# Performance work log

Hardware: AMD Instinct MI355X
Metric: run time of the kernel (lower is better)

The kernel has to match this reference:

```python
import jax, jax.numpy as jnp
import numpy as np

B, P, H, W = 64, 50000, 512, 512


def setup_inputs() -> dict:
    key = jax.random.key(0)
    ks = jax.random.split(key, 6)
    x = jax.random.normal(ks[0], (B, 1, H, W), dtype=jnp.float32)
    x_A = jax.random.randint(ks[1], (B, P), 0, W, dtype=jnp.int32)
    y_A = jax.random.randint(ks[2], (B, P), 0, H, dtype=jnp.int32)
    x_B = jax.random.randint(ks[3], (B, P), 0, W, dtype=jnp.int32)
    y_B = jax.random.randint(ks[4], (B, P), 0, H, dtype=jnp.int32)
    # ordinal relation in {-1, 0, 1}: -1/+1 = ordered pair, 0 = equal depth
    gt = jax.random.randint(ks[5], (B, P), -1, 2).astype(jnp.float32)
    return {"x": x, "x_A": x_A, "y_A": y_A, "x_B": x_B, "y_B": y_B, "gt": gt}


def reference(x, x_A, y_A, x_B, y_B, gt):
    # x: [B,1,H,W] predicted depth; gather z values at sparse point pairs.
    img = x[:, 0]                              # [B,H,W]
    b = jnp.arange(B)[:, None]                 # [B,1] batch index for gather
    z_A = img[b, y_A, x_A]                     # [B,P]
    z_B = img[b, y_B, x_B]                     # [B,P]
    d = z_A - z_B
    mask = jnp.abs(gt)                         # 1 for ordered pairs, 0 for equal
    # ranking loss log(1+exp(-gt*d)) for ordered pairs, (d)^2 for equal pairs
    loss = mask * jnp.log1p(jnp.exp(-gt * d)) + (1.0 - mask) * d * d
    n_point_total = B * P
    return jnp.sum(loss) / n_point_total
```

## Files before the change

### kernel.cpp

```cpp
#include <hip/hip_runtime.h>

#define THREADS 256
#define BLOCKS_PER_XCD 391
#define NXCD 8
#define NBLOCKS (BLOCKS_PER_XCD * NXCD)

typedef int   intx4   __attribute__((ext_vector_type(4)));
typedef float floatx4 __attribute__((ext_vector_type(4)));

__global__ __launch_bounds__(THREADS) void rdc_kernel(
    const float* __restrict__ x,
    const int*   __restrict__ xA,
    const int*   __restrict__ yA,
    const int*   __restrict__ xB,
    const int*   __restrict__ yB,
    const float* __restrict__ gt,
    float* __restrict__ out,
    float inv_n)
{
    const int UPB = 12500;
    const int HW  = 512 * 512;

    const int xcd = blockIdx.x & 7;
    const int lb  = blockIdx.x >> 3;
    const int tlocal = lb * THREADS + threadIdx.x;

    float acc = 0.0f;
    if (tlocal < 8 * UPB) {
        const int bl = tlocal / UPB;
        const int i  = tlocal - bl * UPB;
        const int b  = xcd * 8 + bl;
        const int v  = b * UPB + i;

        const intx4  xa = __builtin_nontemporal_load((const intx4*)xA + v);
        const intx4  ya = __builtin_nontemporal_load((const intx4*)yA + v);
        const intx4  xb = __builtin_nontemporal_load((const intx4*)xB + v);
        const intx4  yb = __builtin_nontemporal_load((const intx4*)yB + v);
        const floatx4 g = __builtin_nontemporal_load((const floatx4*)gt + v);

        const float* __restrict__ img = x + (size_t)b * HW;

        float zA[4], zB[4];
        #pragma unroll
        for (int k = 0; k < 4; ++k) {
            zA[k] = img[(ya[k] << 9) + xa[k]];
            zB[k] = img[(yb[k] << 9) + xb[k]];
        }

        #pragma unroll
        for (int k = 0; k < 4; ++k) {
            float gi = g[k];
            float d  = zA[k] - zB[k];
            float t  = -gi * d;
            float sp = fmaxf(t, 0.0f) + log1pf(__expf(-fabsf(t)));
            float m  = fabsf(gi);
            acc += m * sp + (1.0f - m) * d * d;
        }
    }

    #pragma unroll
    for (int off = 32; off > 0; off >>= 1)
        acc += __shfl_down(acc, off, 64);

    __shared__ float wsum[THREADS / 64];
    const int lane = threadIdx.x & 63;
    const int wid  = threadIdx.x >> 6;
    if (lane == 0) wsum[wid] = acc;
    __syncthreads();
    if (threadIdx.x == 0) {
        float s = 0.0f;
        #pragma unroll
        for (int i2 = 0; i2 < THREADS / 64; ++i2) s += wsum[i2];
        atomicAdd(out, s * inv_n);
    }
}

extern "C" void kernel_launch(void* const* d_in, const int* in_sizes, int n_in,
                              void* d_out, int out_size, void* d_ws, size_t ws_size,
                              hipStream_t stream) {
    const float* x  = (const float*)d_in[0];
    const int*   xA = (const int*)d_in[1];
    const int*   yA = (const int*)d_in[2];
    const int*   xB = (const int*)d_in[3];
    const int*   yB = (const int*)d_in[4];
    const float* gt = (const float*)d_in[5];
    float* out = (float*)d_out;

    const int n = in_sizes[1];
    const float inv_n = 1.0f / (float)n;

    hipMemsetAsync(out, 0, sizeof(float), stream);
    rdc_kernel<<<NBLOCKS, THREADS, 0, stream>>>(x, xA, yA, xB, yB, gt, out, inv_n);
}
```

Before: 172.9 us.

## Stage image bands in LDS and resolve gathers from shared memory

```diff
diff --git a/kernel.cpp b/kernel.cpp
--- a/kernel.cpp
+++ b/kernel.cpp
@@ -1,14 +1,13 @@
 #include <hip/hip_runtime.h>
 
-#define THREADS 256
-#define BLOCKS_PER_XCD 391
-#define NXCD 8
-#define NBLOCKS (BLOCKS_PER_XCD * NXCD)
+#define THREADS 1024
+#define PPT 16
+#define CPB (THREADS * PPT)
+#define NCHUNK 4
+#define NBANDS 16
+#define BAND_F (32 * 512)
 
-typedef int   intx4   __attribute__((ext_vector_type(4)));
-typedef float floatx4 __attribute__((ext_vector_type(4)));
-
-__global__ __launch_bounds__(THREADS) void rdc_kernel(
+__global__ __launch_bounds__(THREADS, 4) void rdc_kernel(
     const float* __restrict__ x,
     const int*   __restrict__ xA,
     const int*   __restrict__ yA,
@@ -18,59 +17,76 @@
     float* __restrict__ out,
     float inv_n)
 {
-    const int UPB = 12500;
-    const int HW  = 512 * 512;
+    __shared__ float band[BAND_F];
+    __shared__ float wsum[THREADS / 64];
 
+    const int tid = threadIdx.x;
     const int xcd = blockIdx.x & 7;
-    const int lb  = blockIdx.x >> 3;
-    const int tlocal = lb * THREADS + threadIdx.x;
+    const int w   = blockIdx.x >> 3;
+    const int bl  = w >> 2;
+    const int ch  = w & 3;
+    const int b   = xcd * 8 + bl;
+    const int base = ch * CPB;
+    const int cnt  = min(CPB, 50000 - base);
+
+    const size_t pbase = (size_t)b * 50000 + base;
+
+    unsigned pa[PPT], pb[PPT];
+    float g[PPT], zA[PPT], zB[PPT];
+    #pragma unroll
+    for (int k = 0; k < PPT; ++k) {
+        const int s = k * THREADS + tid;
+        if (s < cnt) {
+            const size_t p = pbase + s;
+            const int xa_ = __builtin_nontemporal_load(xA + p);
+            const int ya_ = __builtin_nontemporal_load(yA + p);
+            const int xb_ = __builtin_nontemporal_load(xB + p);
+            const int yb_ = __builtin_nontemporal_load(yB + p);
+            g[k]  = __builtin_nontemporal_load(gt + p);
+            pa[k] = (unsigned)((ya_ << 9) | xa_);
+            pb[k] = (unsigned)((yb_ << 9) | xb_);
+        } else {
+            pa[k] = 0xFFFFFFFFu; pb[k] = 0xFFFFFFFFu; g[k] = 0.0f;
+        }
+        zA[k] = 0.0f; zB[k] = 0.0f;
+    }
+
+    const float4* __restrict__ img4 = (const float4*)(x + (size_t)b * (512 * 512));
+
+    for (int bi = 0; bi < NBANDS; ++bi) {
+        __syncthreads();
+        float4* dst4 = (float4*)band;
+        #pragma unroll
+        for (int j = 0; j < BAND_F / 4 / THREADS; ++j)
+            dst4[j * THREADS + tid] = img4[bi * (BAND_F / 4) + j * THREADS + tid];
+        __syncthreads();
+        #pragma unroll
+        for (int k = 0; k < PPT; ++k) {
+            if ((pa[k] >> 14) == (unsigned)bi) zA[k] = band[pa[k] & 16383];
+            if ((pb[k] >> 14) == (unsigned)bi) zB[k] = band[pb[k] & 16383];
+        }
+    }
 
     float acc = 0.0f;
-    if (tlocal < 8 * UPB) {
-        const int bl = tlocal / UPB;
-        const int i  = tlocal - bl * UPB;
-        const int b  = xcd * 8 + bl;
-        const int v  = b * UPB + i;
-
-        const intx4  xa = __builtin_nontemporal_load((const intx4*)xA + v);
-        const intx4  ya = __builtin_nontemporal_load((const intx4*)yA + v);
-        const intx4  xb = __builtin_nontemporal_load((const intx4*)xB + v);
-        const intx4  yb = __builtin_nontemporal_load((const intx4*)yB + v);
-        const floatx4 g = __builtin_nontemporal_load((const floatx4*)gt + v);
-
-        const float* __restrict__ img = x + (size_t)b * HW;
-
-        float zA[4], zB[4];
-        #pragma unroll
-        for (int k = 0; k < 4; ++k) {
-            zA[k] = img[(ya[k] << 9) + xa[k]];
-            zB[k] = img[(yb[k] << 9) + xb[k]];
-        }
-
-        #pragma unroll
-        for (int k = 0; k < 4; ++k) {
-            float gi = g[k];
-            float d  = zA[k] - zB[k];
-            float t  = -gi * d;
-            float sp = fmaxf(t, 0.0f) + log1pf(__expf(-fabsf(t)));
-            float m  = fabsf(gi);
-            acc += m * sp + (1.0f - m) * d * d;
-        }
+    #pragma unroll
+    for (int k = 0; k < PPT; ++k) {
+        const float d = zA[k] - zB[k];
+        const float t = -g[k] * d;
+        const float sp = fmaxf(t, 0.0f) + log1pf(__expf(-fabsf(t)));
+        const float m  = fabsf(g[k]);
+        acc += m * sp + (1.0f - m) * d * d;
     }
 
     #pragma unroll
     for (int off = 32; off > 0; off >>= 1)
         acc += __shfl_down(acc, off, 64);
-
-    __shared__ float wsum[THREADS / 64];
-    const int lane = threadIdx.x & 63;
-    const int wid  = threadIdx.x >> 6;
+    const int lane = tid & 63, wid = tid >> 6;
     if (lane == 0) wsum[wid] = acc;
     __syncthreads();
-    if (threadIdx.x == 0) {
+    if (tid == 0) {
         float s = 0.0f;
         #pragma unroll
-        for (int i2 = 0; i2 < THREADS / 64; ++i2) s += wsum[i2];
+        for (int i = 0; i < THREADS / 64; ++i) s += wsum[i];
         atomicAdd(out, s * inv_n);
     }
 }
@@ -90,5 +106,5 @@
     const float inv_n = 1.0f / (float)n;
 
     hipMemsetAsync(out, 0, sizeof(float), stream);
-    rdc_kernel<<<NBLOCKS, THREADS, 0, stream>>>(x, xA, yA, xB, yB, gt, out, inv_n);
+    rdc_kernel<<<64 * NCHUNK, THREADS, 0, stream>>>(x, xA, yA, xB, yB, gt, out, inv_n);
 }
```

Measured after the change: 188.2 us. 8.8% more time.

## Assign each thread one point across eight batches with software-pipelined gathers

Applied to the files above, without the earlier changes.

```diff
diff --git a/kernel.cpp b/kernel.cpp
--- a/kernel.cpp
+++ b/kernel.cpp
@@ -1,14 +1,10 @@
 #include <hip/hip_runtime.h>
 
 #define THREADS 256
-#define BLOCKS_PER_XCD 391
-#define NXCD 8
-#define NBLOCKS (BLOCKS_PER_XCD * NXCD)
+#define BLOCKS_PER_XCD 196
+#define NBLOCKS (BLOCKS_PER_XCD * 8)
 
-typedef int   intx4   __attribute__((ext_vector_type(4)));
-typedef float floatx4 __attribute__((ext_vector_type(4)));
-
-__global__ __launch_bounds__(THREADS) void rdc_kernel(
+__global__ __launch_bounds__(THREADS, 4) void rdc_kernel(
     const float* __restrict__ x,
     const int*   __restrict__ xA,
     const int*   __restrict__ yA,
@@ -18,43 +14,63 @@
     float* __restrict__ out,
     float inv_n)
 {
-    const int UPB = 12500;
-    const int HW  = 512 * 512;
+    const int HW = 512 * 512;
+    const int P  = 50000;
 
     const int xcd = blockIdx.x & 7;
     const int lb  = blockIdx.x >> 3;
-    const int tlocal = lb * THREADS + threadIdx.x;
+    const int t   = lb * THREADS + threadIdx.x;
 
     float acc = 0.0f;
-    if (tlocal < 8 * UPB) {
-        const int bl = tlocal / UPB;
-        const int i  = tlocal - bl * UPB;
-        const int b  = xcd * 8 + bl;
-        const int v  = b * UPB + i;
+    if (t < P) {
+        const int b0 = xcd * 8;
+        const float* __restrict__ img = x + (size_t)b0 * HW;
+        const size_t pb = (size_t)b0 * P + t;
 
-        const intx4  xa = __builtin_nontemporal_load((const intx4*)xA + v);
-        const intx4  ya = __builtin_nontemporal_load((const intx4*)yA + v);
-        const intx4  xb = __builtin_nontemporal_load((const intx4*)xB + v);
-        const intx4  yb = __builtin_nontemporal_load((const intx4*)yB + v);
-        const floatx4 g = __builtin_nontemporal_load((const floatx4*)gt + v);
+        int   xa0, ya0, xb0, yb0;  float g0;
+        int   xa1, ya1, xb1, yb1;  float g1;
+        float zA0, zB0;
 
-        const float* __restrict__ img = x + (size_t)b * HW;
-
-        float zA[4], zB[4];
-        #pragma unroll
-        for (int k = 0; k < 4; ++k) {
-            zA[k] = img[(ya[k] << 9) + xa[k]];
-            zB[k] = img[(yb[k] << 9) + xb[k]];
-        }
+        xa0 = __builtin_nontemporal_load(xA + pb);
+        ya0 = __builtin_nontemporal_load(yA + pb);
+        xb0 = __builtin_nontemporal_load(xB + pb);
+        yb0 = __builtin_nontemporal_load(yB + pb);
+        g0  = __builtin_nontemporal_load(gt + pb);
+        xa1 = __builtin_nontemporal_load(xA + pb + P);
+        ya1 = __builtin_nontemporal_load(yA + pb + P);
+        xb1 = __builtin_nontemporal_load(xB + pb + P);
+        yb1 = __builtin_nontemporal_load(yB + pb + P);
+        g1  = __builtin_nontemporal_load(gt + pb + P);
+        zA0 = img[(ya0 << 9) + xa0];
+        zB0 = img[(yb0 << 9) + xb0];
 
         #pragma unroll
-        for (int k = 0; k < 4; ++k) {
-            float gi = g[k];
-            float d  = zA[k] - zB[k];
-            float t  = -gi * d;
-            float sp = fmaxf(t, 0.0f) + log1pf(__expf(-fabsf(t)));
-            float m  = fabsf(gi);
+        for (int i = 0; i < 8; ++i) {
+            int nxa = 0, nya = 0, nxb = 0, nyb = 0; float ng = 0.0f;
+            if (i + 2 < 8) {
+                const size_t p2 = pb + (size_t)(i + 2) * P;
+                nxa = __builtin_nontemporal_load(xA + p2);
+                nya = __builtin_nontemporal_load(yA + p2);
+                nxb = __builtin_nontemporal_load(xB + p2);
+                nyb = __builtin_nontemporal_load(yB + p2);
+                ng  = __builtin_nontemporal_load(gt + p2);
+            }
+            float nzA = 0.0f, nzB = 0.0f;
+            if (i + 1 < 8) {
+                const float* __restrict__ img1 = img + HW;
+                nzA = img1[(ya1 << 9) + xa1];
+                nzB = img1[(yb1 << 9) + xb1];
+            }
+            const float d  = zA0 - zB0;
+            const float tt = -g0 * d;
+            const float sp = fmaxf(tt, 0.0f) + log1pf(__expf(-fabsf(tt)));
+            const float m  = fabsf(g0);
             acc += m * sp + (1.0f - m) * d * d;
+
+            img += HW;
+            xa0 = xa1; ya0 = ya1; xb0 = xb1; yb0 = yb1; g0 = g1;
+            xa1 = nxa; ya1 = nya; xb1 = nxb; yb1 = nyb; g1 = ng;
+            zA0 = nzA; zB0 = nzB;
         }
     }
 
```

After: 191.0 us. 10.5% more time.
